# Optimization experiments

Measured on AMD Instinct MI355X. Metric: run time of the kernel, lower is better.

Reference implementation:

```python
import jax, jax.numpy as jnp
import numpy as np

DMODEL, DK, HEADS, FF = 512, 64, 8, 2048
HD = HEADS * DK  # 512; heads are NOT split in this module
EPS = 1e-5


def layernorm(x, g, b):
    mu = jnp.mean(x, axis=-1, keepdims=True)
    var = jnp.mean(jnp.square(x - mu), axis=-1, keepdims=True)
    return (x - mu) * jax.lax.rsqrt(var + EPS) * g + b


def setup_inputs() -> dict:
    key = jax.random.key(0)
    ks = jax.random.split(key, 20)
    s = 1.0 / np.sqrt(DMODEL)
    u = lambda k, shape, fan: jax.random.uniform(k, shape, jnp.float32, -1.0 / np.sqrt(fan), 1.0 / np.sqrt(fan))
    return {
        "x": jax.random.normal(ks[0], (4, 4096, DMODEL), jnp.float32),
        "Wq_w": u(ks[1], (DMODEL, HD), DMODEL), "Wq_b": u(ks[2], (HD,), DMODEL),
        "Wk_w": u(ks[3], (DMODEL, HD), DMODEL), "Wk_b": u(ks[4], (HD,), DMODEL),
        "Wv_w": u(ks[5], (DMODEL, HD), DMODEL), "Wv_b": u(ks[6], (HD,), DMODEL),
        "Wu_w": u(ks[7], (HD, DMODEL), HD), "Wu_b": u(ks[8], (DMODEL,), HD),
        "ln1_g": jnp.ones((DMODEL,), jnp.float32), "ln1_b": jnp.zeros((DMODEL,), jnp.float32),
        "ff1_w": u(ks[9], (DMODEL, FF), DMODEL), "ff1_b": u(ks[10], (FF,), DMODEL),
        "ff2_w": u(ks[11], (FF, DMODEL), FF), "ff2_b": u(ks[12], (DMODEL,), FF),
        "ln2_g": jnp.ones((DMODEL,), jnp.float32), "ln2_b": jnp.zeros((DMODEL,), jnp.float32),
    }


def reference(x, Wq_w, Wq_b, Wk_w, Wk_b, Wv_w, Wv_b, Wu_w, Wu_b,
              ln1_g, ln1_b, ff1_w, ff1_b, ff2_w, ff2_b, ln2_g, ln2_b):
    # x: (b, n, dmodel). Single encoder layer, faithful to num_encoders=1.
    q = x @ Wq_w + Wq_b            # (b, n, HD)
    k = x @ Wk_w + Wk_b
    v = x @ Wv_w + Wv_b
    # NOTE: original does bmm over full HD dim (no head split), scaled by sqrt(dk)
    scores = jnp.einsum('bnd,bmd->bnm', q, k) / np.sqrt(DK)
    probs = jax.nn.softmax(scores, axis=-1)   # (b, n, n) — O(n^2) materialized as in source
    attn = jnp.einsum('bnm,bmd->bnd', probs, v)
    unified = attn @ Wu_w + Wu_b
    h = layernorm(x + unified, ln1_g, ln1_b)
    ffwd = jax.nn.relu(h @ ff1_w + ff1_b) @ ff2_w + ff2_b
    return layernorm(h + ffwd, ln2_g, ln2_b)
```

## Files before the change

### kernel.cpp

```cpp
#include <hip/hip_runtime.h>

#define AS1 __attribute__((address_space(1)))
#define AS3 __attribute__((address_space(3)))

typedef __attribute__((ext_vector_type(8))) short short8;
typedef __attribute__((ext_vector_type(4))) float floatx4;

__device__ __forceinline__ float b2f(ushort u) {
  union { unsigned int i; float f; } x; x.i = ((unsigned int)u) << 16; return x.f;
}
__device__ __forceinline__ ushort f2b(float f) {
  union { float f; unsigned int i; } x; x.f = f;
  unsigned int r = (x.i + 0x7fffu + ((x.i >> 16) & 1u)) >> 16;
  return (ushort)r;
}

#define GF_RELU 1


__global__ void zero_f32(float* __restrict__ p)
{
  p[blockIdx.x * 256 + threadIdx.x] = 0.f;
}

__global__ __launch_bounds__(256) void gemm_vw(
    const ushort* __restrict__ qkv, const ushort* __restrict__ wut,
    ushort* __restrict__ vwt)
{
  __shared__ __align__(16) ushort As[128 * 32];
  __shared__ __align__(16) ushort Bs[128 * 32];

  const int id = blockIdx.x;
  const int b  = id >> 7;
  const int t  = id & 127;
  const int bx = t & 31;
  const int by = t >> 5;

  const ushort* A  = wut;
  const ushort* Bt = qkv + (size_t)b * 4096 * 1536 + 1024;
  ushort* C = vwt + (size_t)b * 512 * 4096;

  const int tid  = threadIdx.x;
  const int w    = tid >> 6;
  const int lane = tid & 63;
  const int lo   = lane & 15;
  const int quad = lane >> 4;
  const int m0   = by * 128;
  const int n0   = bx * 128;
  const int wm   = (w & 1) * 64;
  const int wn   = (w >> 1) * 64;

  const int i0 = tid, i1 = tid + 256;
  const ushort* ga0 = A  + (size_t)(m0 + (i0 >> 2)) * 512 + ((i0 & 3) << 3);
  const ushort* ga1 = A  + (size_t)(m0 + (i1 >> 2)) * 512 + ((i1 & 3) << 3);
  const ushort* gb0 = Bt + (size_t)(n0 + (i0 >> 2)) * 1536 + ((i0 & 3) << 3);
  const ushort* gb1 = Bt + (size_t)(n0 + (i1 >> 2)) * 1536 + ((i1 & 3) << 3);

  floatx4 acc[4][4] = {};

  for (int k0 = 0; k0 < 512; k0 += 32) {
    __syncthreads();
    __builtin_amdgcn_global_load_lds((const AS1 void*)(ga0 + k0), (AS3 void*)(As + i0 * 8), 16, 0, 0);
    __builtin_amdgcn_global_load_lds((const AS1 void*)(ga1 + k0), (AS3 void*)(As + i1 * 8), 16, 0, 0);
    __builtin_amdgcn_global_load_lds((const AS1 void*)(gb0 + k0), (AS3 void*)(Bs + i0 * 8), 16, 0, 0);
    __builtin_amdgcn_global_load_lds((const AS1 void*)(gb1 + k0), (AS3 void*)(Bs + i1 * 8), 16, 0, 0);
    __syncthreads();

    short8 af[4], bf[4];
#pragma unroll
    for (int tt = 0; tt < 4; ++tt) {
      af[tt] = *(const short8*)(As + (wm + tt * 16 + lo) * 32 + quad * 8);
      bf[tt] = *(const short8*)(Bs + (wn + tt * 16 + lo) * 32 + quad * 8);
    }
#pragma unroll
    for (int mt = 0; mt < 4; ++mt)
#pragma unroll
      for (int nt = 0; nt < 4; ++nt)
        acc[mt][nt] = __builtin_amdgcn_mfma_f32_16x16x32_bf16(af[mt], bf[nt], acc[mt][nt], 0, 0, 0);
  }

#pragma unroll
  for (int mt = 0; mt < 4; ++mt)
#pragma unroll
    for (int nt = 0; nt < 4; ++nt)
#pragma unroll
      for (int r = 0; r < 4; ++r) {
        const int row = m0 + wm + mt * 16 + quad * 4 + r;
        const int col = n0 + wn + nt * 16 + lo;
        C[(size_t)row * 4096 + col] = f2b(acc[mt][nt][r]);
      }
}

__global__ __launch_bounds__(256) void gemm_qk_exp(
    const ushort* __restrict__ qkv, ushort* __restrict__ P,
    float* __restrict__ rs)
{
  __shared__ __align__(16) ushort As[128 * 32];
  __shared__ __align__(16) ushort Bs[128 * 32];

  const int id = blockIdx.x;
  const int b  = id >> 10;
  const int t  = id & 1023;
  const int r8 = t & 7;
  const int s2 = t >> 3;
  const int bx = s2 & 31;
  const int by = r8 + ((s2 >> 5) << 3);

  const ushort* A  = qkv + (size_t)b * 4096 * 1536;
  const ushort* Bt = qkv + (size_t)b * 4096 * 1536 + 512;
  ushort* C = P + (size_t)b * 4096 * 4096;

  const int tid  = threadIdx.x;
  const int w    = tid >> 6;
  const int lane = tid & 63;
  const int lo   = lane & 15;
  const int quad = lane >> 4;
  const int m0   = by * 128;
  const int n0   = bx * 128;
  const int wm   = (w & 1) * 64;
  const int wn   = (w >> 1) * 64;

  const int i0 = tid, i1 = tid + 256;
  const ushort* ga0 = A  + (size_t)(m0 + (i0 >> 2)) * 1536 + ((i0 & 3) << 3);
  const ushort* ga1 = A  + (size_t)(m0 + (i1 >> 2)) * 1536 + ((i1 & 3) << 3);
  const ushort* gb0 = Bt + (size_t)(n0 + (i0 >> 2)) * 1536 + ((i0 & 3) << 3);
  const ushort* gb1 = Bt + (size_t)(n0 + (i1 >> 2)) * 1536 + ((i1 & 3) << 3);

  floatx4 acc[4][4] = {};

  for (int k0 = 0; k0 < 512; k0 += 32) {
    __syncthreads();
    __builtin_amdgcn_global_load_lds((const AS1 void*)(ga0 + k0), (AS3 void*)(As + i0 * 8), 16, 0, 0);
    __builtin_amdgcn_global_load_lds((const AS1 void*)(ga1 + k0), (AS3 void*)(As + i1 * 8), 16, 0, 0);
    __builtin_amdgcn_global_load_lds((const AS1 void*)(gb0 + k0), (AS3 void*)(Bs + i0 * 8), 16, 0, 0);
    __builtin_amdgcn_global_load_lds((const AS1 void*)(gb1 + k0), (AS3 void*)(Bs + i1 * 8), 16, 0, 0);
    __syncthreads();

    short8 af[4], bf[4];
#pragma unroll
    for (int tt = 0; tt < 4; ++tt) {
      af[tt] = *(const short8*)(As + (wm + tt * 16 + lo) * 32 + quad * 8);
      bf[tt] = *(const short8*)(Bs + (wn + tt * 16 + lo) * 32 + quad * 8);
    }
#pragma unroll
    for (int mt = 0; mt < 4; ++mt)
#pragma unroll
      for (int nt = 0; nt < 4; ++nt)
        acc[mt][nt] = __builtin_amdgcn_mfma_f32_16x16x32_bf16(af[mt], bf[nt], acc[mt][nt], 0, 0, 0);
  }

#pragma unroll
  for (int mt = 0; mt < 4; ++mt)
#pragma unroll
    for (int r = 0; r < 4; ++r) {
      const int row = m0 + wm + mt * 16 + quad * 4 + r;
      float esum = 0.f;
#pragma unroll
      for (int nt = 0; nt < 4; ++nt) {
        const int col = n0 + wn + nt * 16 + lo;
        const float e = __expf(acc[mt][nt][r] * 0.125f);
        esum += e;
        C[(size_t)row * 4096 + col] = f2b(e);
      }
      esum += __shfl_xor(esum, 1, 64);
      esum += __shfl_xor(esum, 2, 64);
      esum += __shfl_xor(esum, 4, 64);
      esum += __shfl_xor(esum, 8, 64);
      if (lo == 0) atomicAdd(&rs[(size_t)b * 4096 + row], esum);
    }
}

__global__ __launch_bounds__(256) void gemm_pv_wu(
    const ushort* __restrict__ P, const ushort* __restrict__ vwt,
    const float* __restrict__ rs, const float* __restrict__ bias,
    ushort* __restrict__ uni)
{
  __shared__ __align__(16) ushort As[128 * 64];
  __shared__ __align__(16) ushort Bs[128 * 64];

  const int id  = blockIdx.x;
  const int xcd = id & 7;
  const int s   = id >> 3;
  const int bx  = s & 3;
  const int panel = xcd * 16 + (s >> 2);
  const int b  = panel >> 5;
  const int by = panel & 31;

  const ushort* A  = P   + (size_t)b * 4096 * 4096;
  const ushort* Bt = vwt + (size_t)b * 512 * 4096;

  const int tid  = threadIdx.x;
  const int w    = tid >> 6;
  const int lane = tid & 63;
  const int lo   = lane & 15;
  const int quad = lane >> 4;
  const int m0   = by * 128;
  const int n0   = bx * 128;
  const int wm   = (w & 1) * 64;
  const int wn   = (w >> 1) * 64;

  const ushort* gaP[4]; const ushort* gbP[4];
#pragma unroll
  for (int k = 0; k < 4; ++k) {
    const int s_ = tid + k * 256;
    const int row = s_ >> 3, sl = s_ & 7;
    gaP[k] = A  + (size_t)(m0 + row) * 4096 + ((sl ^ (row & 7)) << 3);
    gbP[k] = Bt + (size_t)(n0 + row) * 4096 + ((sl ^ (row & 7)) << 3);
  }

  floatx4 acc[4][4] = {};

  for (int k0 = 0; k0 < 4096; k0 += 64) {
    __syncthreads();
#pragma unroll
    for (int k = 0; k < 4; ++k) {
      const int s_ = tid + k * 256;
      __builtin_amdgcn_global_load_lds((const AS1 void*)(gaP[k] + k0), (AS3 void*)(As + s_ * 8), 16, 0, 0);
      __builtin_amdgcn_global_load_lds((const AS1 void*)(gbP[k] + k0), (AS3 void*)(Bs + s_ * 8), 16, 0, 0);
    }
    __syncthreads();

#pragma unroll
    for (int kk = 0; kk < 2; ++kk) {
      short8 af[4], bf[4];
#pragma unroll
      for (int tt = 0; tt < 4; ++tt) {
        const int ra = wm + tt * 16 + lo;
        const int rb = wn + tt * 16 + lo;
        af[tt] = *(const short8*)(As + (size_t)ra * 64 + (((kk * 4 + quad) ^ (ra & 7)) << 3));
        bf[tt] = *(const short8*)(Bs + (size_t)rb * 64 + (((kk * 4 + quad) ^ (rb & 7)) << 3));
      }
#pragma unroll
      for (int mt = 0; mt < 4; ++mt)
#pragma unroll
        for (int nt = 0; nt < 4; ++nt)
          acc[mt][nt] = __builtin_amdgcn_mfma_f32_16x16x32_bf16(af[mt], bf[nt], acc[mt][nt], 0, 0, 0);
    }
  }

#pragma unroll
  for (int mt = 0; mt < 4; ++mt)
#pragma unroll
    for (int r = 0; r < 4; ++r) {
      const int row = m0 + wm + mt * 16 + quad * 4 + r;
      const size_t grow = (size_t)b * 4096 + row;
      const float inv = 1.f / rs[grow];
#pragma unroll
      for (int nt = 0; nt < 4; ++nt) {
        const int col = n0 + wn + nt * 16 + lo;
        uni[grow * 512 + col] = f2b(acc[mt][nt][r] * inv + bias[col]);
      }
    }
}

__global__ __launch_bounds__(256) void gemm_async(
    const ushort* __restrict__ A, const ushort* __restrict__ Bt,
    const float* __restrict__ bias, ushort* __restrict__ C,
    int N, int K, int lda, int ldb,
    int lg_gx, int lg_gy, float scale, int flags)
{
  __shared__ __align__(16) ushort As[128 * 32];
  __shared__ __align__(16) ushort Bs[128 * 32];

  const int id = blockIdx.x;
  const int r8 = id & 7;
  const int s  = id >> 3;
  const int bx = s & ((1 << lg_gx) - 1);
  const int j  = r8 + ((s >> lg_gx) << 3);
  const int by = j & ((1 << lg_gy) - 1);

  const int tid  = threadIdx.x;
  const int w    = tid >> 6;
  const int lane = tid & 63;
  const int lo   = lane & 15;
  const int quad = lane >> 4;
  const int m0   = by * 128;
  const int n0   = bx * 128;
  const int wm   = (w & 1) * 64;
  const int wn   = (w >> 1) * 64;

  const int i0 = tid, i1 = tid + 256;
  const ushort* ga0 = A  + (size_t)(m0 + (i0 >> 2)) * lda + ((i0 & 3) << 3);
  const ushort* ga1 = A  + (size_t)(m0 + (i1 >> 2)) * lda + ((i1 & 3) << 3);
  const ushort* gb0 = Bt + (size_t)(n0 + (i0 >> 2)) * ldb + ((i0 & 3) << 3);
  const ushort* gb1 = Bt + (size_t)(n0 + (i1 >> 2)) * ldb + ((i1 & 3) << 3);

  floatx4 acc[4][4] = {};

  for (int k0 = 0; k0 < K; k0 += 32) {
    __syncthreads();
    __builtin_amdgcn_global_load_lds((const AS1 void*)(ga0 + k0), (AS3 void*)(As + i0 * 8), 16, 0, 0);
    __builtin_amdgcn_global_load_lds((const AS1 void*)(ga1 + k0), (AS3 void*)(As + i1 * 8), 16, 0, 0);
    __builtin_amdgcn_global_load_lds((const AS1 void*)(gb0 + k0), (AS3 void*)(Bs + i0 * 8), 16, 0, 0);
    __builtin_amdgcn_global_load_lds((const AS1 void*)(gb1 + k0), (AS3 void*)(Bs + i1 * 8), 16, 0, 0);
    __syncthreads();

    short8 af[4], bf[4];
#pragma unroll
    for (int t = 0; t < 4; ++t) {
      af[t] = *(const short8*)(As + (wm + t * 16 + lo) * 32 + quad * 8);
      bf[t] = *(const short8*)(Bs + (wn + t * 16 + lo) * 32 + quad * 8);
    }
#pragma unroll
    for (int mt = 0; mt < 4; ++mt)
#pragma unroll
      for (int nt = 0; nt < 4; ++nt)
        acc[mt][nt] = __builtin_amdgcn_mfma_f32_16x16x32_bf16(af[mt], bf[nt], acc[mt][nt], 0, 0, 0);
  }

#pragma unroll
  for (int mt = 0; mt < 4; ++mt)
#pragma unroll
    for (int nt = 0; nt < 4; ++nt)
#pragma unroll
      for (int r = 0; r < 4; ++r) {
        int row = m0 + wm + mt * 16 + quad * 4 + r;
        int col = n0 + wn + nt * 16 + lo;
        float v = acc[mt][nt][r] * scale;
        if (bias) v += bias[col];
        if (flags & GF_RELU) v = fmaxf(v, 0.f);
        C[(size_t)row * N + col] = f2b(v);
      }
}

__global__ __launch_bounds__(256) void gemm_sync_f32a(
    const float* __restrict__ Af, const ushort* __restrict__ Bt,
    const float* __restrict__ bias, ushort* __restrict__ C,
    int N, int K)
{
  __shared__ __align__(16) ushort As[128 * 32];
  __shared__ __align__(16) ushort Bs[128 * 32];

  const int tid  = threadIdx.x;
  const int w    = tid >> 6;
  const int lane = tid & 63;
  const int lo   = lane & 15;
  const int quad = lane >> 4;
  const int m0   = blockIdx.y * 128;
  const int n0   = blockIdx.x * 128;
  const int wm   = (w & 1) * 64;
  const int wn   = (w >> 1) * 64;

  const int i0 = tid, i1 = tid + 256;
  const size_t aoff0 = (size_t)(m0 + (i0 >> 2)) * K + ((i0 & 3) << 3);
  const size_t aoff1 = (size_t)(m0 + (i1 >> 2)) * K + ((i1 & 3) << 3);
  const size_t boff0 = (size_t)(n0 + (i0 >> 2)) * K + ((i0 & 3) << 3);
  const size_t boff1 = (size_t)(n0 + (i1 >> 2)) * K + ((i1 & 3) << 3);

  floatx4 acc[4][4] = {};

  for (int k0 = 0; k0 < K; k0 += 32) {
    short8 va0, va1;
    const float4 a00 = *(const float4*)(Af + aoff0 + k0);
    const float4 a01 = *(const float4*)(Af + aoff0 + k0 + 4);
    const float4 a10 = *(const float4*)(Af + aoff1 + k0);
    const float4 a11 = *(const float4*)(Af + aoff1 + k0 + 4);
    va0[0] = (short)f2b(a00.x); va0[1] = (short)f2b(a00.y);
    va0[2] = (short)f2b(a00.z); va0[3] = (short)f2b(a00.w);
    va0[4] = (short)f2b(a01.x); va0[5] = (short)f2b(a01.y);
    va0[6] = (short)f2b(a01.z); va0[7] = (short)f2b(a01.w);
    va1[0] = (short)f2b(a10.x); va1[1] = (short)f2b(a10.y);
    va1[2] = (short)f2b(a10.z); va1[3] = (short)f2b(a10.w);
    va1[4] = (short)f2b(a11.x); va1[5] = (short)f2b(a11.y);
    va1[6] = (short)f2b(a11.z); va1[7] = (short)f2b(a11.w);
    const short8 vb0 = *(const short8*)(Bt + boff0 + k0);
    const short8 vb1 = *(const short8*)(Bt + boff1 + k0);
    __syncthreads();
    *(short8*)(As + i0 * 8) = va0;
    *(short8*)(As + i1 * 8) = va1;
    *(short8*)(Bs + i0 * 8) = vb0;
    *(short8*)(Bs + i1 * 8) = vb1;
    __syncthreads();

    short8 af[4], bf[4];
#pragma unroll
    for (int t = 0; t < 4; ++t) {
      af[t] = *(const short8*)(As + (wm + t * 16 + lo) * 32 + quad * 8);
      bf[t] = *(const short8*)(Bs + (wn + t * 16 + lo) * 32 + quad * 8);
    }
#pragma unroll
    for (int mt = 0; mt < 4; ++mt)
#pragma unroll
      for (int nt = 0; nt < 4; ++nt)
        acc[mt][nt] = __builtin_amdgcn_mfma_f32_16x16x32_bf16(af[mt], bf[nt], acc[mt][nt], 0, 0, 0);
  }

#pragma unroll
  for (int mt = 0; mt < 4; ++mt)
#pragma unroll
    for (int nt = 0; nt < 4; ++nt)
#pragma unroll
      for (int r = 0; r < 4; ++r) {
        int row = m0 + wm + mt * 16 + quad * 4 + r;
        int col = n0 + wn + nt * 16 + lo;
        C[(size_t)row * N + col] = f2b(acc[mt][nt][r] + bias[col]);
      }
}

__global__ void transpose_cast(const float* __restrict__ in, ushort* __restrict__ out,
                               int R, int C)
{
  __shared__ ushort t[64][65];
  const int r0 = blockIdx.y * 64, c0 = blockIdx.x * 64;
  const int tx = threadIdx.x, ty = threadIdx.y;
  for (int i = ty; i < 64; i += 4)
    t[i][tx] = f2b(in[(size_t)(r0 + i) * C + c0 + tx]);
  __syncthreads();
  for (int i = ty; i < 64; i += 4)
    out[(size_t)(c0 + i) * R + r0 + tx] = t[tx][i];
}

__global__ void concat_bias(const float* __restrict__ a, const float* __restrict__ b,
                            const float* __restrict__ c, float* __restrict__ o)
{
  const int i = blockIdx.x * 256 + threadIdx.x;
  o[i] = (i < 512) ? a[i] : ((i < 1024) ? b[i - 512] : c[i - 1024]);
}

__global__ __launch_bounds__(256) void ln_res(
    const void* __restrict__ Xv, int x_f32, const ushort* __restrict__ Y,
    const float* __restrict__ g, const float* __restrict__ b,
    void* __restrict__ outv, int o_f32)
{
  const int w = threadIdx.x >> 6, lane = threadIdx.x & 63;
  const size_t row = (size_t)blockIdx.x * 4 + w;
  const size_t base = row * 512 + lane * 8;

  float v[8];
  if (x_f32) {
    const float* X = (const float*)Xv + base;
    const float4 x0 = *(const float4*)(X), x1 = *(const float4*)(X + 4);
    v[0] = x0.x; v[1] = x0.y; v[2] = x0.z; v[3] = x0.w;
    v[4] = x1.x; v[5] = x1.y; v[6] = x1.z; v[7] = x1.w;
  } else {
    const short8 xv = *(const short8*)((const ushort*)Xv + base);
#pragma unroll
    for (int j = 0; j < 8; ++j) v[j] = b2f((ushort)xv[j]);
  }
  const short8 yv = *(const short8*)(Y + base);
  float s = 0.f, sq = 0.f;
#pragma unroll
  for (int j = 0; j < 8; ++j) {
    v[j] += b2f((ushort)yv[j]);
    s += v[j]; sq += v[j] * v[j];
  }
  for (int m = 1; m < 64; m <<= 1) {
    s  += __shfl_xor(s,  m, 64);
    sq += __shfl_xor(sq, m, 64);
  }
  const float mean = s * (1.f / 512.f);
  const float var  = sq * (1.f / 512.f) - mean * mean;
  const float rstd = rsqrtf(fmaxf(var, 0.f) + 1e-5f);

  const float4 g0 = *(const float4*)(g + lane * 8);
  const float4 g1 = *(const float4*)(g + lane * 8 + 4);
  const float4 b0 = *(const float4*)(b + lane * 8);
  const float4 b1 = *(const float4*)(b + lane * 8 + 4);
  const float gg[8] = {g0.x, g0.y, g0.z, g0.w, g1.x, g1.y, g1.z, g1.w};
  const float bb[8] = {b0.x, b0.y, b0.z, b0.w, b1.x, b1.y, b1.z, b1.w};

  if (o_f32) {
    float* o = (float*)outv + base;
#pragma unroll
    for (int j = 0; j < 8; ++j) o[j] = (v[j] - mean) * rstd * gg[j] + bb[j];
  } else {
    ushort* o = (ushort*)outv + base;
    short8 ov;
#pragma unroll
    for (int j = 0; j < 8; ++j) ov[j] = (short)f2b((v[j] - mean) * rstd * gg[j] + bb[j]);
    *(short8*)o = ov;
  }
}

extern "C" void kernel_launch(void* const* d_in, const int* in_sizes, int n_in,
                              void* d_out, int out_size, void* d_ws, size_t ws_size,
                              hipStream_t stream)
{
  const float* x    = (const float*)d_in[0];
  const float* Wq_w = (const float*)d_in[1];
  const float* Wq_b = (const float*)d_in[2];
  const float* Wk_w = (const float*)d_in[3];
  const float* Wk_b = (const float*)d_in[4];
  const float* Wv_w = (const float*)d_in[5];
  const float* Wv_b = (const float*)d_in[6];
  const float* Wu_w = (const float*)d_in[7];
  const float* Wu_b = (const float*)d_in[8];
  const float* g1   = (const float*)d_in[9];
  const float* b1   = (const float*)d_in[10];
  const float* f1w  = (const float*)d_in[11];
  const float* f1b  = (const float*)d_in[12];
  const float* f2w  = (const float*)d_in[13];
  const float* f2bv = (const float*)d_in[14];
  const float* g2   = (const float*)d_in[15];
  const float* b2   = (const float*)d_in[16];

  char* wsb = (char*)d_ws;
  ushort* wqkvt = (ushort*)(wsb + 0);
  ushort* wut   = (ushort*)(wsb + 1572864);
  ushort* f1t   = (ushort*)(wsb + 2097152);
  ushort* f2t   = (ushort*)(wsb + 4194304);
  float*  bqkv  = (float*) (wsb + 6291456);
  ushort* qkv   = (ushort*)(wsb + 6297600);
  ushort* vwt   = (ushort*)(wsb + 56629248);
  ushort* uni   = (ushort*)(wsb + 73406464);
  ushort* h     = (ushort*)(wsb + 106960896);
  ushort* mid   = (ushort*)(wsb + 123738112);
  ushort* ffo   = (ushort*)(wsb + 190846976);
  float*  rowsum = (float*)(wsb + 0);
  ushort* Pbuf   = (ushort*)(wsb + 90183680);

  const dim3 tb(64, 4);
  transpose_cast<<<dim3(8, 8),  tb, 0, stream>>>(Wq_w, wqkvt,              512, 512);
  transpose_cast<<<dim3(8, 8),  tb, 0, stream>>>(Wk_w, wqkvt + 512 * 512,  512, 512);
  transpose_cast<<<dim3(8, 8),  tb, 0, stream>>>(Wv_w, wqkvt + 1024 * 512, 512, 512);
  transpose_cast<<<dim3(8, 8),  tb, 0, stream>>>(Wu_w, wut, 512, 512);
  transpose_cast<<<dim3(32, 8), tb, 0, stream>>>(f1w, f1t, 512, 2048);
  transpose_cast<<<dim3(8, 32), tb, 0, stream>>>(f2w, f2t, 2048, 512);
  concat_bias<<<6, 256, 0, stream>>>(Wq_b, Wk_b, Wv_b, bqkv);

  gemm_sync_f32a<<<dim3(12, 128), 256, 0, stream>>>(x, wqkvt, bqkv, qkv, 1536, 512);

  zero_f32<<<64, 256, 0, stream>>>(rowsum);
  gemm_vw<<<512, 256, 0, stream>>>(qkv, wut, vwt);
  gemm_qk_exp<<<4096, 256, 0, stream>>>(qkv, Pbuf, rowsum);
  gemm_pv_wu<<<512, 256, 0, stream>>>(Pbuf, vwt, rowsum, Wu_b, uni);

  ln_res<<<4096, 256, 0, stream>>>(x, 1, uni, g1, b1, h, 0);

  gemm_async<<<2048, 256, 0, stream>>>(h, f1t, f1b, mid,
      2048, 512, 512, 512, 4, 7, 1.f, GF_RELU);
  gemm_async<<<512, 256, 0, stream>>>(mid, f2t, f2bv, ffo,
      512, 2048, 2048, 2048, 2, 7, 1.f, 0);
  ln_res<<<4096, 256, 0, stream>>>(h, 0, ffo, g2, b2, d_out, 1);
}
```

Before: 564.2 us.

## Compute softmax row sums via MFMA in PV kernel; use BK=64 swizzled tiles

Drops the atomic row-sum accumulation and zero-init kernel from the QK^T exp kernel. The PV kernel now computes each row's denominator by running extra MFMAs of the bf16 P tile against a vector of ones, then normalises from shared memory. The QK and FFN GEMMs also switch to 64-wide K tiles with XOR-swizzled LDS, halving barrier count per K. Row sums now come from bf16-rounded P values rather than fp32 exponentials, which slightly changes numerics. The PV kernel also pays for extra MFMA work.

Result: faster. 512.1 us (-9.2%).

```diff
diff --git a/kernel.cpp b/kernel.cpp
--- a/kernel.cpp
+++ b/kernel.cpp
@@ -17,11 +17,6 @@
 
 #define GF_RELU 1
 
-
-__global__ void zero_f32(float* __restrict__ p)
-{
-  p[blockIdx.x * 256 + threadIdx.x] = 0.f;
-}
 
 __global__ __launch_bounds__(256) void gemm_vw(
     const ushort* __restrict__ qkv, const ushort* __restrict__ wut,
@@ -92,11 +87,10 @@
 }
 
 __global__ __launch_bounds__(256) void gemm_qk_exp(
-    const ushort* __restrict__ qkv, ushort* __restrict__ P,
-    float* __restrict__ rs)
-{
-  __shared__ __align__(16) ushort As[128 * 32];
-  __shared__ __align__(16) ushort Bs[128 * 32];
+    const ushort* __restrict__ qkv, ushort* __restrict__ P)
+{
+  __shared__ __align__(16) ushort As[128 * 64];
+  __shared__ __align__(16) ushort Bs[128 * 64];
 
   const int id = blockIdx.x;
   const int b  = id >> 10;
@@ -120,33 +114,43 @@
   const int wm   = (w & 1) * 64;
   const int wn   = (w >> 1) * 64;
 
-  const int i0 = tid, i1 = tid + 256;
-  const ushort* ga0 = A  + (size_t)(m0 + (i0 >> 2)) * 1536 + ((i0 & 3) << 3);
-  const ushort* ga1 = A  + (size_t)(m0 + (i1 >> 2)) * 1536 + ((i1 & 3) << 3);
-  const ushort* gb0 = Bt + (size_t)(n0 + (i0 >> 2)) * 1536 + ((i0 & 3) << 3);
-  const ushort* gb1 = Bt + (size_t)(n0 + (i1 >> 2)) * 1536 + ((i1 & 3) << 3);
+  const ushort* gaP[4]; const ushort* gbP[4];
+#pragma unroll
+  for (int k = 0; k < 4; ++k) {
+    const int s_ = tid + k * 256;
+    const int row = s_ >> 3, sl = s_ & 7;
+    gaP[k] = A  + (size_t)(m0 + row) * 1536 + ((sl ^ (row & 7)) << 3);
+    gbP[k] = Bt + (size_t)(n0 + row) * 1536 + ((sl ^ (row & 7)) << 3);
+  }
 
   floatx4 acc[4][4] = {};
 
-  for (int k0 = 0; k0 < 512; k0 += 32) {
-    __syncthreads();
-    __builtin_amdgcn_global_load_lds((const AS1 void*)(ga0 + k0), (AS3 void*)(As + i0 * 8), 16, 0, 0);
-    __builtin_amdgcn_global_load_lds((const AS1 void*)(ga1 + k0), (AS3 void*)(As + i1 * 8), 16, 0, 0);
-    __builtin_amdgcn_global_load_lds((const AS1 void*)(gb0 + k0), (AS3 void*)(Bs + i0 * 8), 16, 0, 0);
-    __builtin_amdgcn_global_load_lds((const AS1 void*)(gb1 + k0), (AS3 void*)(Bs + i1 * 8), 16, 0, 0);
-    __syncthreads();
-
-    short8 af[4], bf[4];
-#pragma unroll
-    for (int tt = 0; tt < 4; ++tt) {
-      af[tt] = *(const short8*)(As + (wm + tt * 16 + lo) * 32 + quad * 8);
-      bf[tt] = *(const short8*)(Bs + (wn + tt * 16 + lo) * 32 + quad * 8);
-    }
-#pragma unroll
-    for (int mt = 0; mt < 4; ++mt)
-#pragma unroll
-      for (int nt = 0; nt < 4; ++nt)
-        acc[mt][nt] = __builtin_amdgcn_mfma_f32_16x16x32_bf16(af[mt], bf[nt], acc[mt][nt], 0, 0, 0);
+  for (int k0 = 0; k0 < 512; k0 += 64) {
+    __syncthreads();
+#pragma unroll
+    for (int k = 0; k < 4; ++k) {
+      const int s_ = tid + k * 256;
+      __builtin_amdgcn_global_load_lds((const AS1 void*)(gaP[k] + k0), (AS3 void*)(As + s_ * 8), 16, 0, 0);
+      __builtin_amdgcn_global_load_lds((const AS1 void*)(gbP[k] + k0), (AS3 void*)(Bs + s_ * 8), 16, 0, 0);
+    }
+    __syncthreads();
+
+#pragma unroll
+    for (int kk = 0; kk < 2; ++kk) {
+      short8 af[4], bf[4];
+#pragma unroll
+      for (int tt = 0; tt < 4; ++tt) {
+        const int ra = wm + tt * 16 + lo;
+        const int rb = wn + tt * 16 + lo;
+        af[tt] = *(const short8*)(As + (size_t)ra * 64 + (((kk * 4 + quad) ^ (ra & 7)) << 3));
+        bf[tt] = *(const short8*)(Bs + (size_t)rb * 64 + (((kk * 4 + quad) ^ (rb & 7)) << 3));
+      }
+#pragma unroll
+      for (int mt = 0; mt < 4; ++mt)
+#pragma unroll
+        for (int nt = 0; nt < 4; ++nt)
+          acc[mt][nt] = __builtin_amdgcn_mfma_f32_16x16x32_bf16(af[mt], bf[nt], acc[mt][nt], 0, 0, 0);
+    }
   }
 
 #pragma unroll
@@ -154,29 +158,21 @@
 #pragma unroll
     for (int r = 0; r < 4; ++r) {
       const int row = m0 + wm + mt * 16 + quad * 4 + r;
-      float esum = 0.f;
 #pragma unroll
       for (int nt = 0; nt < 4; ++nt) {
         const int col = n0 + wn + nt * 16 + lo;
-        const float e = __expf(acc[mt][nt][r] * 0.125f);
-        esum += e;
-        C[(size_t)row * 4096 + col] = f2b(e);
-      }
-      esum += __shfl_xor(esum, 1, 64);
-      esum += __shfl_xor(esum, 2, 64);
-      esum += __shfl_xor(esum, 4, 64);
-      esum += __shfl_xor(esum, 8, 64);
-      if (lo == 0) atomicAdd(&rs[(size_t)b * 4096 + row], esum);
+        C[(size_t)row * 4096 + col] = f2b(__expf(acc[mt][nt][r] * 0.125f));
+      }
     }
 }
 
 __global__ __launch_bounds__(256) void gemm_pv_wu(
     const ushort* __restrict__ P, const ushort* __restrict__ vwt,
-    const float* __restrict__ rs, const float* __restrict__ bias,
-    ushort* __restrict__ uni)
+    const float* __restrict__ bias, ushort* __restrict__ uni)
 {
   __shared__ __align__(16) ushort As[128 * 64];
   __shared__ __align__(16) ushort Bs[128 * 64];
+  __shared__ float rsm[128];
 
   const int id  = blockIdx.x;
   const int xcd = id & 7;
@@ -208,7 +204,12 @@
     gbP[k] = Bt + (size_t)(n0 + row) * 4096 + ((sl ^ (row & 7)) << 3);
   }
 
+  short8 ones;
+#pragma unroll
+  for (int j = 0; j < 8; ++j) ones[j] = (short)0x3F80;
+
   floatx4 acc[4][4] = {};
+  floatx4 rsacc[4] = {};
 
   for (int k0 = 0; k0 < 4096; k0 += 64) {
     __syncthreads();
@@ -231,6 +232,9 @@
         bf[tt] = *(const short8*)(Bs + (size_t)rb * 64 + (((kk * 4 + quad) ^ (rb & 7)) << 3));
       }
 #pragma unroll
+      for (int tt = 0; tt < 4; ++tt)
+        rsacc[tt] = __builtin_amdgcn_mfma_f32_16x16x32_bf16(af[tt], ones, rsacc[tt], 0, 0, 0);
+#pragma unroll
       for (int mt = 0; mt < 4; ++mt)
 #pragma unroll
         for (int nt = 0; nt < 4; ++nt)
@@ -238,13 +242,22 @@
     }
   }
 
+  if (wn == 0 && lo == 0) {
+#pragma unroll
+    for (int tt = 0; tt < 4; ++tt)
+#pragma unroll
+      for (int r = 0; r < 4; ++r)
+        rsm[wm + tt * 16 + quad * 4 + r] = rsacc[tt][r];
+  }
+  __syncthreads();
+
 #pragma unroll
   for (int mt = 0; mt < 4; ++mt)
 #pragma unroll
     for (int r = 0; r < 4; ++r) {
-      const int row = m0 + wm + mt * 16 + quad * 4 + r;
-      const size_t grow = (size_t)b * 4096 + row;
-      const float inv = 1.f / rs[grow];
+      const int lrow = wm + mt * 16 + quad * 4 + r;
+      const size_t grow = (size_t)b * 4096 + m0 + lrow;
+      const float inv = 1.f / rsm[lrow];
 #pragma unroll
       for (int nt = 0; nt < 4; ++nt) {
         const int col = n0 + wn + nt * 16 + lo;
@@ -253,14 +266,14 @@
     }
 }
 
-__global__ __launch_bounds__(256) void gemm_async(
+__global__ __launch_bounds__(256) void gemm_async64(
     const ushort* __restrict__ A, const ushort* __restrict__ Bt,
     const float* __restrict__ bias, ushort* __restrict__ C,
     int N, int K, int lda, int ldb,
     int lg_gx, int lg_gy, float scale, int flags)
 {
-  __shared__ __align__(16) ushort As[128 * 32];
-  __shared__ __align__(16) ushort Bs[128 * 32];
+  __shared__ __align__(16) ushort As[128 * 64];
+  __shared__ __align__(16) ushort Bs[128 * 64];
 
   const int id = blockIdx.x;
   const int r8 = id & 7;
@@ -279,33 +292,43 @@
   const int wm   = (w & 1) * 64;
   const int wn   = (w >> 1) * 64;
 
-  const int i0 = tid, i1 = tid + 256;
-  const ushort* ga0 = A  + (size_t)(m0 + (i0 >> 2)) * lda + ((i0 & 3) << 3);
-  const ushort* ga1 = A  + (size_t)(m0 + (i1 >> 2)) * lda + ((i1 & 3) << 3);
-  const ushort* gb0 = Bt + (size_t)(n0 + (i0 >> 2)) * ldb + ((i0 & 3) << 3);
-  const ushort* gb1 = Bt + (size_t)(n0 + (i1 >> 2)) * ldb + ((i1 & 3) << 3);
+  const ushort* gaP[4]; const ushort* gbP[4];
+#pragma unroll
+  for (int k = 0; k < 4; ++k) {
+    const int s_ = tid + k * 256;
+    const int row = s_ >> 3, sl = s_ & 7;
+    gaP[k] = A  + (size_t)(m0 + row) * lda + ((sl ^ (row & 7)) << 3);
+    gbP[k] = Bt + (size_t)(n0 + row) * ldb + ((sl ^ (row & 7)) << 3);
+  }
 
   floatx4 acc[4][4] = {};
 
-  for (int k0 = 0; k0 < K; k0 += 32) {
-    __syncthreads();
-    __builtin_amdgcn_global_load_lds((const AS1 void*)(ga0 + k0), (AS3 void*)(As + i0 * 8), 16, 0, 0);
-    __builtin_amdgcn_global_load_lds((const AS1 void*)(ga1 + k0), (AS3 void*)(As + i1 * 8), 16, 0, 0);
-    __builtin_amdgcn_global_load_lds((const AS1 void*)(gb0 + k0), (AS3 void*)(Bs + i0 * 8), 16, 0, 0);
-    __builtin_amdgcn_global_load_lds((const AS1 void*)(gb1 + k0), (AS3 void*)(Bs + i1 * 8), 16, 0, 0);
-    __syncthreads();
-
-    short8 af[4], bf[4];
-#pragma unroll
-    for (int t = 0; t < 4; ++t) {
-      af[t] = *(const short8*)(As + (wm + t * 16 + lo) * 32 + quad * 8);
-      bf[t] = *(const short8*)(Bs + (wn + t * 16 + lo) * 32 + quad * 8);
-    }
-#pragma unroll
-    for (int mt = 0; mt < 4; ++mt)
-#pragma unroll
-      for (int nt = 0; nt < 4; ++nt)
-        acc[mt][nt] = __builtin_amdgcn_mfma_f32_16x16x32_bf16(af[mt], bf[nt], acc[mt][nt], 0, 0, 0);
+  for (int k0 = 0; k0 < K; k0 += 64) {
+    __syncthreads();
+#pragma unroll
+    for (int k = 0; k < 4; ++k) {
+      const int s_ = tid + k * 256;
+      __builtin_amdgcn_global_load_lds((const AS1 void*)(gaP[k] + k0), (AS3 void*)(As + s_ * 8), 16, 0, 0);
+      __builtin_amdgcn_global_load_lds((const AS1 void*)(gbP[k] + k0), (AS3 void*)(Bs + s_ * 8), 16, 0, 0);
+    }
+    __syncthreads();
+
+#pragma unroll
+    for (int kk = 0; kk < 2; ++kk) {
+      short8 af[4], bf[4];
+#pragma unroll
+      for (int tt = 0; tt < 4; ++tt) {
+        const int ra = wm + tt * 16 + lo;
+        const int rb = wn + tt * 16 + lo;
+        af[tt] = *(const short8*)(As + (size_t)ra * 64 + (((kk * 4 + quad) ^ (ra & 7)) << 3));
+        bf[tt] = *(const short8*)(Bs + (size_t)rb * 64 + (((kk * 4 + quad) ^ (rb & 7)) << 3));
+      }
+#pragma unroll
+      for (int mt = 0; mt < 4; ++mt)
+#pragma unroll
+        for (int nt = 0; nt < 4; ++nt)
+          acc[mt][nt] = __builtin_amdgcn_mfma_f32_16x16x32_bf16(af[mt], bf[nt], acc[mt][nt], 0, 0, 0);
+    }
   }
 
 #pragma unroll
@@ -506,8 +529,7 @@
   ushort* h     = (ushort*)(wsb + 106960896);
   ushort* mid   = (ushort*)(wsb + 123738112);
   ushort* ffo   = (ushort*)(wsb + 190846976);
-  float*  rowsum = (float*)(wsb + 0);
-  ushort* Pbuf   = (ushort*)(wsb + 90183680);
+  ushort* Pbuf  = (ushort*)(wsb + 90183680);
 
   const dim3 tb(64, 4);
   transpose_cast<<<dim3(8, 8),  tb, 0, stream>>>(Wq_w, wqkvt,              512, 512);
@@ -520,16 +542,15 @@
 
   gemm_sync_f32a<<<dim3(12, 128), 256, 0, stream>>>(x, wqkvt, bqkv, qkv, 1536, 512);
 
-  zero_f32<<<64, 256, 0, stream>>>(rowsum);
   gemm_vw<<<512, 256, 0, stream>>>(qkv, wut, vwt);
-  gemm_qk_exp<<<4096, 256, 0, stream>>>(qkv, Pbuf, rowsum);
-  gemm_pv_wu<<<512, 256, 0, stream>>>(Pbuf, vwt, rowsum, Wu_b, uni);
+  gemm_qk_exp<<<4096, 256, 0, stream>>>(qkv, Pbuf);
+  gemm_pv_wu<<<512, 256, 0, stream>>>(Pbuf, vwt, Wu_b, uni);
 
   ln_res<<<4096, 256, 0, stream>>>(x, 1, uni, g1, b1, h, 0);
 
-  gemm_async<<<2048, 256, 0, stream>>>(h, f1t, f1b, mid,
+  gemm_async64<<<2048, 256, 0, stream>>>(h, f1t, f1b, mid,
       2048, 512, 512, 512, 4, 7, 1.f, GF_RELU);
-  gemm_async<<<512, 256, 0, stream>>>(mid, f2t, f2bv, ffo,
+  gemm_async64<<<512, 256, 0, stream>>>(mid, f2t, f2bv, ffo,
       512, 2048, 2048, 2048, 2, 7, 1.f, 0);
   ln_res<<<4096, 256, 0, stream>>>(h, 0, ffo, g2, b2, d_out, 1);
 }
```
